# Performance work log

Hardware: AMD Instinct MI355X
Metric: run time of the kernel (lower is better)

## Reference

```python
import jax, jax.numpy as jnp
import numpy as np


def _layer_norm(x, g, b, eps=1e-5):
    mu = x.mean(-1, keepdims=True)
    var = ((x - mu) ** 2).mean(-1, keepdims=True)
    return (x - mu) * jax.lax.rsqrt(var + eps) * g + b


def _linear(x, w, b):
    # torch nn.Linear: y = x @ W^T + b, w has shape (out, in)
    return jnp.einsum('...i,oi->...o', x, w) + b


def setup_inputs() -> dict:
    key = jax.random.key(0)
    ks = jax.random.split(key, 12)
    B, N, C = 1, 512, 128
    s = 0.02  # weight init scale
    f32 = jnp.float32
    return {
        'X': jax.random.normal(ks[0], (B, N, N, C), f32),
        'mask': jax.random.randint(ks[1], (B, N, N, 1), 0, 2) > 0,
        # first LayerNorm
        'ln1_g': jnp.ones((C,), f32), 'ln1_b': jnp.zeros((C,), f32),
        # left edge MLP: Linear -> Sigmoid -> Linear
        'lw1': jax.random.normal(ks[2], (C, C), f32) * s, 'lb1': jnp.zeros((C,), f32),
        'lw2': jax.random.normal(ks[3], (C, C), f32) * s, 'lb2': jnp.zeros((C,), f32),
        # right edge MLP
        'rw1': jax.random.normal(ks[4], (C, C), f32) * s, 'rb1': jnp.zeros((C,), f32),
        'rw2': jax.random.normal(ks[5], (C, C), f32) * s, 'rb2': jnp.zeros((C,), f32),
        # skip gate: Linear -> Sigmoid
        'sw': jax.random.normal(ks[6], (C, C), f32) * s, 'sb': jnp.zeros((C,), f32),
        # combine: LayerNorm -> Linear
        'ln2_g': jnp.ones((C,), f32), 'ln2_b': jnp.zeros((C,), f32),
        'cw': jax.random.normal(ks[7], (C, C), f32) * s, 'cb': jnp.zeros((C,), f32),
    }


def reference(X, mask, ln1_g, ln1_b, lw1, lb1, lw2, lb2,
              rw1, rb1, rw2, rb2, sw, sb, ln2_g, ln2_b, cw, cb):
    h = _layer_norm(X, ln1_g, ln1_b)                      # (B,N,N,C)
    A = _linear(jax.nn.sigmoid(_linear(h, lw1, lb1)), lw2, lb2)
    Bm = _linear(jax.nn.sigmoid(_linear(h, rw1, rb1)), rw2, rb2)
    G = jax.nn.sigmoid(_linear(h, sw, sb))
    A = jnp.where(mask, A, 0.0)
    Bm = jnp.where(mask, Bm, 0.0)
    # triangle multiplication, 'outgoing': contract over k per channel
    T = jnp.einsum('bikc,bjkc->bijc', A, Bm)              # (B,N,N,C)
    Y = _linear(_layer_norm(T, ln2_g, ln2_b), cw, cb) * G
    return Y
```

## Files before the change

kernel.cpp:

```cpp
#include <hip/hip_runtime.h>

typedef unsigned short u16;
typedef unsigned int   u32;
typedef u32   u32x4  __attribute__((ext_vector_type(4)));
typedef __bf16 bf16x8 __attribute__((ext_vector_type(8)));
typedef float f32x4  __attribute__((ext_vector_type(4)));

#define NPOS (512*512)
#define WSLOT 16384

__device__ __forceinline__ u16 f2bf(float f){
  __bf16 h=(__bf16)f;
  return __builtin_bit_cast(u16,h);
}
__device__ __forceinline__ float bf2f(u16 s){ u32 u=((u32)s)<<16; return __builtin_bit_cast(float,u); }
union pk8 { u16 s[8]; u32x4 v; };

__device__ __forceinline__ void gload16(const void* g, void* l){
  __builtin_amdgcn_global_load_lds((const __attribute__((address_space(1))) void*)g,
                                   (__attribute__((address_space(3))) void*)l, 16, 0, 0);
}

__device__ __forceinline__ bf16x8 cvt8(const float* p){
  f32x4 w0=*(const f32x4*)p, w1=*(const f32x4*)(p+4);
  bf16x8 b;
#pragma unroll
  for(int e=0;e<4;e++){ b[e]=(__bf16)w0[e]; b[4+e]=(__bf16)w1[e]; }
  return b;
}

__global__ __launch_bounds__(256) void k0(
    const float* __restrict__ lw1, const float* __restrict__ lw2,
    const float* __restrict__ rw1, const float* __restrict__ rw2,
    const float* __restrict__ sw,  const float* __restrict__ cw, u16* __restrict__ Wp)
{
  const float* srcs[6]={lw1,lw2,rw1,rw2,sw,cw};
  const float* W=srcs[blockIdx.x];
  u16* dst=Wp + (size_t)blockIdx.x*WSLOT;
  const int t=threadIdx.x, lane=t&63, wvv=t>>6, lr=lane&15, quad=lane>>4;
#pragma unroll
  for(int i=0;i<8;i++){
    int tile=wvv*8+i, nt=tile>>2, kk=tile&3;
    const float* p=W+(size_t)(nt*16+lr)*128+kk*32+quad*8;
    bf16x8 b=cvt8(p);
    *(u32x4*)(dst+((size_t)tile*64+lane)*8)=__builtin_bit_cast(u32x4,b);
  }
}

__device__ __forceinline__ void wave_gemm2(const u16 (*sh)[136], int wv, int lane,
    const u16* __restrict__ Wp, const float* __restrict__ bias, float o[4][2][4])
{
  const int lr=lane&15, quad=lane>>4;
  bf16x8 b[2][4];
#pragma unroll
  for(int n2=0;n2<2;n2++){
    const int nt=wv*2+n2;
#pragma unroll
    for(int kk=0;kk<4;kk++)
      b[n2][kk]=*(const bf16x8*)(Wp+((size_t)((nt*4+kk)*64+lane))*8);
  }
  float bv[2]={bias[(wv*2)*16+lr], bias[(wv*2+1)*16+lr]};
#pragma unroll
  for(int mt=0;mt<4;mt++){
    bf16x8 a[4];
#pragma unroll
    for(int kk=0;kk<4;kk++) a[kk]=*(const bf16x8*)&sh[mt*16+lr][kk*32+quad*8];
#pragma unroll
    for(int n2=0;n2<2;n2++){
      f32x4 acc={0.f,0.f,0.f,0.f};
#pragma unroll
      for(int kk=0;kk<4;kk++)
        acc=__builtin_amdgcn_mfma_f32_16x16x32_bf16(a[kk],b[n2][kk],acc,0,0,0);
#pragma unroll
      for(int r=0;r<4;r++) o[mt][n2][r]=acc[r]+bv[n2];
    }
  }
}

__device__ __forceinline__ void sig_to_lds2(u16 (*sh)[136], int wv,int lane, float o[4][2][4]){
  const int lr=lane&15, quad=lane>>4;
#pragma unroll
  for(int mt=0;mt<4;mt++)
#pragma unroll
    for(int n2=0;n2<2;n2++)
#pragma unroll
      for(int r=0;r<4;r++)
        sh[mt*16+quad*4+r][(wv*2+n2)*16+lr]=f2bf(1.f/(1.f+__expf(-o[mt][n2][r])));
}

__device__ __forceinline__ void mask_to_lds2(u16 (*sh)[136], int wv,int lane, float o[4][2][4], const float* smask){
  const int lr=lane&15, quad=lane>>4;
#pragma unroll
  for(int mt=0;mt<4;mt++)
#pragma unroll
    for(int n2=0;n2<2;n2++)
#pragma unroll
      for(int r=0;r<4;r++){
        int row=mt*16+quad*4+r;
        sh[row][(wv*2+n2)*16+lr]=f2bf(o[mt][n2][r]*smask[row]);
      }
}

__device__ __forceinline__ void store_tr(const u16 (*sh)[136], int t, u16* __restrict__ dst, int p0){
#pragma unroll
  for(int iter=0;iter<4;iter++){
    int c=iter*32+(t>>3);
    int pos=(t&7)*8;
    pk8 u;
#pragma unroll
    for(int r=0;r<8;r++){
      int rp=(r+(t>>3)+(t&7))&7;
      u.s[rp]=sh[pos+rp][c];
    }
    *(u32x4*)(dst+(size_t)c*NPOS+p0+pos)=u.v;
  }
}

__global__ __launch_bounds__(256,4) void k1(
    const float* __restrict__ X, const void* __restrict__ mask,
    const float* __restrict__ g1, const float* __restrict__ b1,
    const u16* __restrict__ Wp,
    const float* __restrict__ lb1, const float* __restrict__ lb2,
    const float* __restrict__ rb1, const float* __restrict__ rb2,
    const float* __restrict__ sb,
    u16* __restrict__ At, u16* __restrict__ Bt,
    u16* __restrict__ Gb, float* __restrict__ Gf, int gb16)
{
  __shared__ u16 shh[64][136];
  __shared__ u16 sht[64][136];
  __shared__ float smask[64];
  __shared__ int mpacked;
  const int t=threadIdx.x;
  const int p0=blockIdx.x*64;
  if(t==0){
    const int* m32=(const int*)mask;
    int pk=0;
#pragma unroll
    for(int i=0;i<32;i++){ u32 v=(u32)m32[i]; if(v>1u) pk=1; }
    mpacked=pk;
  }
  {
    int row=t>>2, q=t&3;
    const float* xp = X + (size_t)(p0+row)*128 + q*32;
    float v[32]; float s=0.f,s2=0.f;
#pragma unroll
    for(int u=0;u<8;u++){ f32x4 d=*(const f32x4*)(xp+u*4);
#pragma unroll
      for(int e=0;e<4;e++) v[u*4+e]=d[e]; }
#pragma unroll
    for(int i=0;i<32;i++){ s+=v[i]; s2+=v[i]*v[i]; }
    s+=__shfl_xor(s,1); s2+=__shfl_xor(s2,1);
    s+=__shfl_xor(s,2); s2+=__shfl_xor(s2,2);
    float mu=s*(1.f/128.f);
    float rstd=1.f/sqrtf(s2*(1.f/128.f)-mu*mu+1e-5f);
#pragma unroll
    for(int u=0;u<4;u++){
      pk8 o;
#pragma unroll
      for(int e=0;e<8;e++){
        int c=q*32+u*8+e;
        o.s[e]=f2bf((v[u*8+e]-mu)*rstd*g1[c]+b1[c]);
      }
      *(u32x4*)&shh[row][q*32+u*8]=o.v;
    }
  }
  __syncthreads();
  if(t<64){
    int p=p0+t;
    int mval = mpacked ? (int)((const unsigned char*)mask)[p] : ((const int*)mask)[p];
    smask[t]=(mval!=0)?1.f:0.f;
  }
  const int lane=t&63, wv=t>>6;
  float oL[4][2][4], oR[4][2][4];
  wave_gemm2(shh,wv,lane,Wp+0*WSLOT,lb1,oL);
  sig_to_lds2(sht,wv,lane,oL);
  __syncthreads();
  wave_gemm2(sht,wv,lane,Wp+1*WSLOT,lb2,oL);
  __syncthreads();
  mask_to_lds2(sht,wv,lane,oL,smask);
  __syncthreads();
  store_tr(sht,t,At,p0);
  wave_gemm2(shh,wv,lane,Wp+2*WSLOT,rb1,oR);
  __syncthreads();
  sig_to_lds2(sht,wv,lane,oR);
  __syncthreads();
  wave_gemm2(sht,wv,lane,Wp+3*WSLOT,rb2,oR);
  __syncthreads();
  mask_to_lds2(sht,wv,lane,oR,smask);
  __syncthreads();
  store_tr(sht,t,Bt,p0);
  wave_gemm2(shh,wv,lane,Wp+4*WSLOT,sb,oL);
  const int lr=lane&15, quad=lane>>4;
#pragma unroll
  for(int mt=0;mt<4;mt++)
#pragma unroll
    for(int n2=0;n2<2;n2++)
#pragma unroll
      for(int r=0;r<4;r++){
        size_t p=p0+mt*16+quad*4+r;
        float sg=1.f/(1.f+__expf(-oL[mt][n2][r]));
        size_t idx=p*128+(wv*2+n2)*16+lr;
        if(gb16) Gb[idx]=f2bf(sg); else Gf[idx]=sg;
      }
}

__global__ __launch_bounds__(256) void k2(const u16* __restrict__ At, const u16* __restrict__ Bt,
                                          u16* __restrict__ T, int j_base, int jc, int nxsh)
{
  __shared__ u16 sA[2][8192];
  __shared__ u16 sB[2][8192];
  const int t=threadIdx.x, lane=t&63, wv=t>>6;
  const int bid=blockIdx.x;
  const int tpcsh=2+nxsh;
  const int xcd=bid&7, q=bid>>3;
  const int c   = xcd*16 + (q>>tpcsh);
  const int tile= q & ((1<<tpcsh)-1);
  const int j0l = (tile & ((1<<nxsh)-1))*128;
  const int i0  = (tile >> nxsh)*128;
  const int wm=(wv>>1)*64, wn=(wv&1)*64, lr=lane&15, quad=lane>>4;
  const u16* Ab = At + (size_t)c*NPOS + (size_t)i0*512;
  const u16* Bb = Bt + (size_t)c*NPOS + (size_t)(j_base+j0l)*512;
  const int srow = lane>>3;
  const int scol = ((lane&7) ^ srow)*8;
  const int swz  = (lr&7)<<4;

  f32x4 acc[4][4];
#pragma unroll
  for(int i=0;i<4;i++)
#pragma unroll
    for(int j=0;j<4;j++) acc[i][j]=(f32x4){0.f,0.f,0.f,0.f};

#define K2_STAGE(buf,k0) {                                              \
    _Pragma("unroll")                                                   \
    for(int j=0;j<4;j++){                                               \
      int seg=wv*4+j;                                                   \
      int row=seg*8+srow;                                               \
      gload16(Ab + (size_t)row*512 + (k0) + scol, &sA[buf][seg*512]);   \
      gload16(Bb + (size_t)row*512 + (k0) + scol, &sB[buf][seg*512]);   \
    } }

  K2_STAGE(0,0)
  __syncthreads();
  int cur=0;
  for(int it=0; it<8; ++it){
    if(it<7) K2_STAGE(cur^1,(it+1)*64)
    const char* sAc=(const char*)sA[cur];
    const char* sBc=(const char*)sB[cur];
#pragma unroll
    for(int ks=0;ks<2;ks++){
      bf16x8 a[4],b[4];
#pragma unroll
      for(int mt=0;mt<4;mt++){
        int row=wm+mt*16+lr;
        a[mt]=*(const bf16x8*)(sAc + row*128 + ((ks*64+quad*16)^swz));
      }
#pragma unroll
      for(int nt=0;nt<4;nt++){
        int row=wn+nt*16+lr;
        b[nt]=*(const bf16x8*)(sBc + row*128 + ((ks*64+quad*16)^swz));
      }
#pragma unroll
      for(int mt=0;mt<4;mt++)
#pragma unroll
        for(int nt=0;nt<4;nt++)
          acc[mt][nt]=__builtin_amdgcn_mfma_f32_16x16x32_bf16(a[mt],b[nt],acc[mt][nt],0,0,0);
    }
    __syncthreads();
    cur^=1;
  }
#undef K2_STAGE
  u16* Tb = T + (size_t)c*512*jc;
#pragma unroll
  for(int mt=0;mt<4;mt++)
#pragma unroll
    for(int nt=0;nt<4;nt++)
#pragma unroll
      for(int r=0;r<4;r++){
        int row=i0+wm+mt*16+quad*4+r;
        int col=j0l+wn+nt*16+lr;
        Tb[(size_t)row*jc+col]=f2bf(acc[mt][nt][r]);
      }
}

__global__ __launch_bounds__(256) void k3(const u16* __restrict__ T,
    const u16* __restrict__ cwp,
    const float* __restrict__ g2, const float* __restrict__ b2,
    const float* __restrict__ cb,
    const u16* __restrict__ Gb, float* GY,
    int j_base, int jc, int jshift, int gb16)
{
  __shared__ u16 sH[128][136];
  const int t=threadIdx.x;
  const int cp0=blockIdx.x*128;
  {
    int c=t>>1, half=t&1;
    const u16* Tp = T + (size_t)c*512*jc + cp0 + half*64;
#pragma unroll
    for(int u=0;u<8;u++){
      pk8 d; d.v=*(const u32x4*)(Tp+u*8);
#pragma unroll
      for(int e=0;e<8;e++) sH[half*64+u*8+e][c]=d.s[e];
    }
  }
  __syncthreads();
  {
    int pos=t>>1, half=t&1;
    float s=0.f,s2=0.f;
#pragma unroll
    for(int u=0;u<8;u++){
      pk8 d; d.v=*(const u32x4*)&sH[pos][half*64+u*8];
#pragma unroll
      for(int e=0;e<8;e++){ float x=bf2f(d.s[e]); s+=x; s2+=x*x; }
    }
    s+=__shfl_xor(s,1); s2+=__shfl_xor(s2,1);
    float mu=s*(1.f/128.f);
    float rstd=1.f/sqrtf(s2*(1.f/128.f)-mu*mu+1e-5f);
#pragma unroll
    for(int u=0;u<8;u++){
      pk8 d; d.v=*(const u32x4*)&sH[pos][half*64+u*8];
      pk8 o;
#pragma unroll
      for(int e=0;e<8;e++){
        int c=half*64+u*8+e;
        o.s[e]=f2bf((bf2f(d.s[e])-mu)*rstd*g2[c]+b2[c]);
      }
      *(u32x4*)&sH[pos][half*64+u*8]=o.v;
    }
  }
  __syncthreads();
  const int lane=t&63, wv=t>>6, m0=wv*32, lr=lane&15, quad=lane>>4;
  bf16x8 a[2][4];
#pragma unroll
  for(int mt=0;mt<2;mt++)
#pragma unroll
    for(int kk=0;kk<4;kk++) a[mt][kk]=*(const bf16x8*)&sH[m0+mt*16+lr][kk*32+quad*8];
#pragma unroll
  for(int nt=0;nt<8;nt++){
    f32x4 a0={0.f,0.f,0.f,0.f}, a1={0.f,0.f,0.f,0.f};
#pragma unroll
    for(int kk=0;kk<4;kk++){
      bf16x8 b=*(const bf16x8*)(cwp+((size_t)((nt*4+kk)*64+lane))*8);
      a0=__builtin_amdgcn_mfma_f32_16x16x32_bf16(a[0][kk],b,a0,0,0,0);
      a1=__builtin_amdgcn_mfma_f32_16x16x32_bf16(a[1][kk],b,a1,0,0,0);
    }
    float cbv=cb[nt*16+lr];
#pragma unroll
    for(int mt=0;mt<2;mt++){
      f32x4 ac = mt? a1: a0;
#pragma unroll
      for(int r=0;r<4;r++){
        int l=m0+mt*16+quad*4+r;
        int pl=cp0+l;
        size_t p=((size_t)(pl>>jshift)<<9)+(size_t)j_base+(pl&(jc-1));
        int col=nt*16+lr;
        size_t idx=p*128+col;
        if(gb16){
          GY[idx]=(ac[r]+cbv)*bf2f(Gb[idx]);
        }else{
          float gg=GY[idx];
          GY[idx]=(ac[r]+cbv)*gg;
        }
      }
    }
  }
}

__global__ void kprobe(float* out, u32 wsmib){
  if(threadIdx.x==0 && blockIdx.x==0) out[0]=(float)wsmib;
}

extern "C" void kernel_launch(void* const* d_in, const int* in_sizes, int n_in,
                              void* d_out, int out_size, void* d_ws, size_t ws_size,
                              hipStream_t stream)
{
  (void)in_sizes; (void)n_in; (void)out_size;
  const float* X  =(const float*)d_in[0];
  const void*  mask=d_in[1];
  const float* g1 =(const float*)d_in[2];  const float* b1 =(const float*)d_in[3];
  const float* lw1=(const float*)d_in[4];  const float* lb1=(const float*)d_in[5];
  const float* lw2=(const float*)d_in[6];  const float* lb2=(const float*)d_in[7];
  const float* rw1=(const float*)d_in[8];  const float* rb1=(const float*)d_in[9];
  const float* rw2=(const float*)d_in[10]; const float* rb2=(const float*)d_in[11];
  const float* sw =(const float*)d_in[12]; const float* sb =(const float*)d_in[13];
  const float* g2 =(const float*)d_in[14]; const float* b2 =(const float*)d_in[15];
  const float* cw =(const float*)d_in[16]; const float* cb =(const float*)d_in[17];
  float* out=(float*)d_out;

  const size_t wbytes = (size_t)6*WSLOT*sizeof(u16);
  const size_t szAB   = 2*(size_t)NPOS*128*sizeof(u16);
  const size_t szG    = (size_t)NPOS*128*sizeof(u16);
  const size_t base   = wbytes + szAB;
  int jc=0, jshift=0, nxsh=0, gb=0;
  if      (ws_size >= base + (size_t)512*512*128*2 + szG){ jc=512; jshift=9; nxsh=2; gb=1; }
  else if (ws_size >= base + (size_t)512*512*128*2)      { jc=512; jshift=9; nxsh=2; gb=0; }
  else if (ws_size >= base + (size_t)512*256*128*2 + szG){ jc=256; jshift=8; nxsh=1; gb=1; }
  else if (ws_size >= base + (size_t)512*256*128*2)      { jc=256; jshift=8; nxsh=1; gb=0; }
  else if (ws_size >= base + (size_t)512*128*128*2 + szG){ jc=128; jshift=7; nxsh=0; gb=1; }
  else if (ws_size >= base + (size_t)512*128*128*2)      { jc=128; jshift=7; nxsh=0; gb=0; }
  if(jc==0){
    kprobe<<<dim3(1),dim3(64),0,stream>>>(out,(u32)(ws_size>>20));
    return;
  }
  u16* Wp=(u16*)d_ws;
  u16* At=Wp+(size_t)6*WSLOT;
  u16* Bt=At+(size_t)NPOS*128;
  u16* T =Bt+(size_t)NPOS*128;
  u16* Gb=T +(size_t)512*jc*128;

  k0<<<dim3(6),dim3(256),0,stream>>>(lw1,lw2,rw1,rw2,sw,cw,Wp);
  k1<<<dim3(4096),dim3(256),0,stream>>>(X,mask,g1,b1,Wp,lb1,lb2,rb1,rb2,sb,At,Bt,Gb,out,gb);
  const int nbl=(jc/128)*4*128;
  for(int jb=0;jb<512;jb+=jc){
    k2<<<dim3(nbl),dim3(256),0,stream>>>(At,Bt,T,jb,jc,nxsh);
    k3<<<dim3(4*jc),dim3(256),0,stream>>>(T,Wp+(size_t)5*WSLOT,g2,b2,cb,Gb,out,jb,jc,jshift,gb);
  }
}
```

Baseline: 570.2 us.

## Store T in chunked position-major layout and single-buffer k2 LDS

Changes the T intermediate layout so each block of 128 positions holds all 128 channels contiguously, making k3's loads contiguous instead of strided across channels. Also replaces k2's double-buffered LDS staging with a single buffer and two barriers per k-step, halving LDS use. This trades away overlap between global loads and MFMA compute for possibly higher occupancy. k2's stores become scattered in 128-element segments per channel.

```diff
diff --git a/kernel.cpp b/kernel.cpp
--- a/kernel.cpp
+++ b/kernel.cpp
@@ -207,8 +207,8 @@
 __global__ __launch_bounds__(256) void k2(const u16* __restrict__ At, const u16* __restrict__ Bt,
                                           u16* __restrict__ T, int j_base, int jc, int nxsh)
 {
-  __shared__ u16 sA[2][8192];
-  __shared__ u16 sB[2][8192];
+  __shared__ u16 sA[128*64];
+  __shared__ u16 sB[128*64];
   const int t=threadIdx.x, lane=t&63, wv=t>>6;
   const int bid=blockIdx.x;
   const int tpcsh=2+nxsh;
@@ -223,29 +223,22 @@
   const int srow = lane>>3;
   const int scol = ((lane&7) ^ srow)*8;
   const int swz  = (lr&7)<<4;
-
   f32x4 acc[4][4];
 #pragma unroll
   for(int i=0;i<4;i++)
 #pragma unroll
     for(int j=0;j<4;j++) acc[i][j]=(f32x4){0.f,0.f,0.f,0.f};
-
-#define K2_STAGE(buf,k0) {                                              \
-    _Pragma("unroll")                                                   \
-    for(int j=0;j<4;j++){                                               \
-      int seg=wv*4+j;                                                   \
-      int row=seg*8+srow;                                               \
-      gload16(Ab + (size_t)row*512 + (k0) + scol, &sA[buf][seg*512]);   \
-      gload16(Bb + (size_t)row*512 + (k0) + scol, &sB[buf][seg*512]);   \
-    } }
-
-  K2_STAGE(0,0)
-  __syncthreads();
-  int cur=0;
-  for(int it=0; it<8; ++it){
-    if(it<7) K2_STAGE(cur^1,(it+1)*64)
-    const char* sAc=(const char*)sA[cur];
-    const char* sBc=(const char*)sB[cur];
+  for(int k0=0;k0<512;k0+=64){
+#pragma unroll
+    for(int j=0;j<4;j++){
+      int seg=wv*4+j;
+      int row=seg*8+srow;
+      gload16(Ab + (size_t)row*512 + k0 + scol, &sA[seg*512]);
+      gload16(Bb + (size_t)row*512 + k0 + scol, &sB[seg*512]);
+    }
+    __syncthreads();
+    const char* sAc=(const char*)sA;
+    const char* sBc=(const char*)sB;
 #pragma unroll
     for(int ks=0;ks<2;ks++){
       bf16x8 a[4],b[4];
@@ -266,10 +259,9 @@
           acc[mt][nt]=__builtin_amdgcn_mfma_f32_16x16x32_bf16(a[mt],b[nt],acc[mt][nt],0,0,0);
     }
     __syncthreads();
-    cur^=1;
-  }
-#undef K2_STAGE
-  u16* Tb = T + (size_t)c*512*jc;
+  }
+  const int jcsh7 = jc>>7;
+  const int coff  = wn + lr;
 #pragma unroll
   for(int mt=0;mt<4;mt++)
 #pragma unroll
@@ -277,8 +269,9 @@
 #pragma unroll
       for(int r=0;r<4;r++){
         int row=i0+wm+mt*16+quad*4+r;
-        int col=j0l+wn+nt*16+lr;
-        Tb[(size_t)row*jc+col]=f2bf(acc[mt][nt][r]);
+        int chunk=row*jcsh7 + (j0l>>7);
+        int off=coff + nt*16;
+        T[(size_t)chunk*16384 + (size_t)c*128 + off]=f2bf(acc[mt][nt][r]);
       }
 }
 
@@ -294,7 +287,7 @@
   const int cp0=blockIdx.x*128;
   {
     int c=t>>1, half=t&1;
-    const u16* Tp = T + (size_t)c*512*jc + cp0 + half*64;
+    const u16* Tp = T + (size_t)blockIdx.x*16384 + (size_t)c*128 + half*64;
 #pragma unroll
     for(int u=0;u<8;u++){
       pk8 d; d.v=*(const u32x4*)(Tp+u*8);
```

Result: no change. 561.5 us (-1.5%).
